# Performance work log

Measured on AMD Instinct MI355X. Metric: run time of the kernel, lower is better.

The kernel has to match this reference:

```python
import jax, jax.numpy as jnp
import numpy as np

EPS = 1e-5  # instance-norm epsilon (NormalizeLayer over spatial axes)

def instance_norm(x):
    # normalize over spatial axes (1,2) per sample, per channel
    mean = jnp.mean(x, axis=(1, 2), keepdims=True)
    var = jnp.var(x, axis=(1, 2), keepdims=True)
    return (x - mean) / jnp.sqrt(var + EPS)

def l2norm(x, axis=-1):
    return x / jnp.sqrt(jnp.sum(x * x, axis=axis, keepdims=True) + 1e-12)

def setup_inputs() -> dict:
    key = jax.random.key(0)
    ks = jax.random.split(key, 5)
    B, H, W, C = 4, 64, 64, 256
    content = jax.random.normal(ks[0], (B, H, W, C), jnp.float32)
    style = jax.random.normal(ks[1], (B, H, W, C), jnp.float32)
    scale = 1.0 / np.sqrt(C)
    Wq = jax.random.normal(ks[2], (C, C), jnp.float32) * scale
    Wk = jax.random.normal(ks[3], (C, C), jnp.float32) * scale
    Wv = jax.random.normal(ks[4], (C, C), jnp.float32) * scale
    bq = jnp.zeros((C,), jnp.float32)
    bk = jnp.zeros((C,), jnp.float32)
    bv = jnp.zeros((C,), jnp.float32)
    return {"content": content, "style": style, "Wq": Wq, "bq": bq,
            "Wk": Wk, "bk": bk, "Wv": Wv, "bv": bv}

def reference(content, style, Wq, bq, Wk, bk, Wv, bv):
    B, H, W, C = content.shape
    N = H * W
    norm_content = instance_norm(content)
    norm_style = instance_norm(style)
    # 1x1 convs == per-pixel linear layers
    Q = (jnp.einsum('bhwc,cd->bhwd', norm_content, Wq) + bq).reshape(B, N, C)
    K = (jnp.einsum('bhwc,cd->bhwd', norm_style, Wk) + bk).reshape(B, N, C)
    V = (jnp.einsum('bhwc,cd->bhwd', style, Wv) + bv).reshape(B, N, C)
    # cosine-similarity attention (Dot with normalize=True)
    attn = jnp.einsum('bnc,bmc->bnm', l2norm(Q), l2norm(K))  # [B, N, N]
    A = jax.nn.softmax(attn, axis=-1)
    M = jnp.einsum('bnm,bmc->bnc', A, V)                 # weighted mean
    S2 = jnp.einsum('bnm,bmc->bnc', A, V * V) - M * M    # weighted variance
    S2 = jax.nn.relu(S2)
    # safe sqrt: grad-safe at exactly 0 (matches sqrt(relu(x)) values)
    S = jnp.where(S2 > 0, jnp.sqrt(jnp.where(S2 > 0, S2, 1.0)), 0.0)
    S = S.reshape(B, H, W, C)
    M = M.reshape(B, H, W, C)
    return S * norm_content + M
```

## Files before the change

### kernel.cpp

```cpp
#include <hip/hip_runtime.h>
#include <cstdint>

#define BB 4
#define NN 4096
#define CC 256

typedef __attribute__((ext_vector_type(8))) short bf16x8;
typedef __attribute__((ext_vector_type(4))) short bf16x4;
typedef __attribute__((ext_vector_type(4))) float f32x4;
typedef unsigned int u32;
typedef __attribute__((ext_vector_type(4))) u32 u32x4;
typedef __attribute__((ext_vector_type(2))) u32 u32x2;

#define MFMA_FP8(a, b, c)  __builtin_amdgcn_mfma_f32_16x16x32_fp8_fp8((a), (b), (c), 0, 0, 0)

#define WAITCNT(vm, xp, lgkm) (((vm) & 0xF) | (((vm) >> 4) << 14) | ((xp) << 4) | ((lgkm) << 8))

__device__ __forceinline__ unsigned short f2bf(float f) {
  union { float f; unsigned u; } v; v.f = f;
  unsigned r = v.u + 0x7fffu + ((v.u >> 16) & 1u);
  return (unsigned short)(r >> 16);
}
__device__ __forceinline__ u32 pk4_fp8(float a, float b, float c, float d) {
  u32 v = (u32)__builtin_amdgcn_cvt_pk_fp8_f32(a, b, 0, false);
  v = (u32)__builtin_amdgcn_cvt_pk_fp8_f32(c, d, (int)v, true);
  return v;
}
__device__ __forceinline__ unsigned char fp8_1(float a) {
  return (unsigned char)(((u32)__builtin_amdgcn_cvt_pk_fp8_f32(a, a, 0, false)) & 0xff);
}

typedef __attribute__((address_space(3))) unsigned int lds_u32;
typedef __attribute__((address_space(1))) unsigned int glb_u32;

__device__ __forceinline__ void async_cp16(const void* g, void* l) {
  __builtin_amdgcn_global_load_lds((const glb_u32*)g,
                                   (lds_u32*)(unsigned)(unsigned long long)l,
                                   16, 0, 0);
}

__global__ __launch_bounds__(256) void transpose_w(const float* __restrict__ Wq,
                                                   const float* __restrict__ Wk,
                                                   const float* __restrict__ Wv,
                                                   unsigned char* __restrict__ Wt8) {
  __shared__ float sT[64 * 65];
  int blk = blockIdx.x;
  int z = blk / 16, tl = blk % 16;
  int c0 = (tl >> 2) * 64, d0 = (tl & 3) * 64;
  const float* W = (z == 0) ? Wq : ((z == 1) ? Wk : Wv);
  #pragma unroll
  for (int i = 0; i < 16; ++i) {
    int e = i * 256 + threadIdx.x;
    int c = e >> 6, d = e & 63;
    sT[c * 65 + d] = W[(size_t)(c0 + c) * CC + d0 + d];
  }
  __syncthreads();
  #pragma unroll
  for (int i = 0; i < 16; ++i) {
    int e = i * 256 + threadIdx.x;
    int d = e >> 6, c = e & 63;
    Wt8[(size_t)z * 65536 + (size_t)(d0 + d) * CC + c0 + c] = fp8_1(sT[c * 65 + d]);
  }
}

__global__ __launch_bounds__(256) void stats_partial(const float* __restrict__ content,
                                                     const float* __restrict__ style,
                                                     float* __restrict__ sums) {
  int blk = blockIdx.x;
  int t = blk >> 9, b = (blk >> 7) & 3, chunk = blk & 127;
  const float* X = t ? style : content;
  int c = threadIdx.x;
  const float* base = X + ((size_t)b * NN + (size_t)chunk * 32) * CC + c;
  float s = 0.f, ss = 0.f;
  #pragma unroll 8
  for (int r = 0; r < 32; ++r) {
    float x = base[(size_t)r * CC];
    s += x; ss += x * x;
  }
  atomicAdd(&sums[((t * 2 + 0) * BB + b) * CC + c], s);
  atomicAdd(&sums[((t * 2 + 1) * BB + b) * CC + c], ss);
}

__global__ __launch_bounds__(256) void stats_finalize(const float* __restrict__ sums,
                                                      float* __restrict__ stats) {
  int i = blockIdx.x * 256 + threadIdx.x;
  int t = i >> 10, bc = i & 1023;
  float s = sums[(t * 2 + 0) * 1024 + bc];
  float ss = sums[(t * 2 + 1) * 1024 + bc];
  float m = s * (1.0f / NN);
  float var = ss * (1.0f / NN) - m * m;
  stats[(t * 2 + 0) * 1024 + bc] = m;
  stats[(t * 2 + 1) * 1024 + bc] = rsqrtf(var + 1e-5f);
}

__global__ __launch_bounds__(256, 2) void qkv_kernel(
    const float* __restrict__ content, const float* __restrict__ style,
    const unsigned char* __restrict__ Wt8,
    const float* __restrict__ bq, const float* __restrict__ bk, const float* __restrict__ bv,
    const float* __restrict__ stats,
    unsigned char* __restrict__ Qn, unsigned char* __restrict__ Kn,
    unsigned char* __restrict__ Vct) {
  __shared__ __align__(16) char sW[32768];
  __shared__ __align__(16) char sX[32768];

  int tid = threadIdx.x;
  int wid = tid >> 6, lane = tid & 63, quad = lane >> 4, l16 = lane & 15;
  int uwid = __builtin_amdgcn_readfirstlane(wid);
  int tileid = blockIdx.x;
  int z = blockIdx.y;
  int gr0 = tileid * 128;
  int b = gr0 >> 12;

  const float* X = (z == 0) ? content : style;
  int statt = (z == 0) ? 0 : 1;
  const float* mean = stats + ((statt * 2 + 0) * BB + b) * CC;
  const float* rstd = stats + ((statt * 2 + 1) * BB + b) * CC;
  bool donorm = (z < 2);

  #pragma unroll
  for (int i = 0; i < 8; ++i) {
    int lin = i * 256 + tid;
    int row = lin >> 4, c16 = lin & 15;
    int c = c16 * 16;
    const float* xr = X + (size_t)(gr0 + row) * CC + c;
    f32x4 x0 = *(const f32x4*)(xr + 0);
    f32x4 x1 = *(const f32x4*)(xr + 4);
    f32x4 x2 = *(const f32x4*)(xr + 8);
    f32x4 x3 = *(const f32x4*)(xr + 12);
    if (donorm) {
      f32x4 m0 = *(const f32x4*)(mean + c + 0), r0 = *(const f32x4*)(rstd + c + 0);
      f32x4 m1 = *(const f32x4*)(mean + c + 4), r1 = *(const f32x4*)(rstd + c + 4);
      f32x4 m2 = *(const f32x4*)(mean + c + 8), r2 = *(const f32x4*)(rstd + c + 8);
      f32x4 m3 = *(const f32x4*)(mean + c + 12), r3 = *(const f32x4*)(rstd + c + 12);
      x0 = (x0 - m0) * r0; x1 = (x1 - m1) * r1;
      x2 = (x2 - m2) * r2; x3 = (x3 - m3) * r3;
    }
    u32x4 pk;
    pk.x = pk4_fp8(x0.x, x0.y, x0.z, x0.w);
    pk.y = pk4_fp8(x1.x, x1.y, x1.z, x1.w);
    pk.z = pk4_fp8(x2.x, x2.y, x2.z, x2.w);
    pk.w = pk4_fp8(x3.x, x3.y, x3.z, x3.w);
    *(u32x4*)(sX + row * 256 + ((c16 ^ (row & 15)) * 16)) = pk;
  }

  f32x4 zero4 = {0.f, 0.f, 0.f, 0.f};
  f32x4 acc[2][16];
  #pragma unroll
  for (int i = 0; i < 2; ++i)
    #pragma unroll
    for (int j = 0; j < 16; ++j) acc[i][j] = zero4;

  const unsigned char* wb = Wt8 + (size_t)z * 65536;

  for (int half = 0; half < 2; ++half) {
    __syncthreads();
    #pragma unroll
    for (int it = 0; it < 8; ++it) {
      int L = it * 256 + wid * 64 + lane;
      int d = L >> 3;
      int c16 = (L & 7) ^ (d & 7);
      async_cp16(wb + (size_t)d * 256 + half * 128 + c16 * 16,
                 sW + (size_t)(it * 256 + uwid * 64) * 16);
    }
    __syncthreads();

    long a[2][4];
    #pragma unroll
    for (int mf = 0; mf < 2; ++mf) {
      int row = wid * 32 + mf * 16 + l16;
      #pragma unroll
      for (int kc = 0; kc < 4; ++kc) {
        int chunk = half * 8 + kc * 2 + (quad >> 1);
        a[mf][kc] = *(const long*)(sX + row * 256 + ((chunk ^ (row & 15)) * 16) + (quad & 1) * 8);
      }
    }
    #pragma unroll
    for (int nf = 0; nf < 16; ++nf) {
      int d = nf * 16 + l16;
      #pragma unroll
      for (int kc = 0; kc < 4; ++kc) {
        long bw = *(const long*)(sW + d * 128 + (((kc * 2 + (quad >> 1)) ^ (d & 7)) * 16) + (quad & 1) * 8);
        acc[0][nf] = MFMA_FP8(a[0][kc], bw, acc[0][nf]);
        acc[1][nf] = MFMA_FP8(a[1][kc], bw, acc[1][nf]);
      }
    }
  }

  const float* bias = (z == 0) ? bq : ((z == 1) ? bk : bv);
  #pragma unroll
  for (int nf = 0; nf < 16; ++nf) {
    float bb_ = bias[nf * 16 + l16];
    #pragma unroll
    for (int mf = 0; mf < 2; ++mf) {
      acc[mf][nf].x += bb_; acc[mf][nf].y += bb_;
      acc[mf][nf].z += bb_; acc[mf][nf].w += bb_;
    }
  }

  if (z < 2) {
    unsigned char* O = (z == 0) ? Qn : Kn;
    #pragma unroll
    for (int mf = 0; mf < 2; ++mf) {
      f32x4 ss = zero4;
      #pragma unroll
      for (int nf = 0; nf < 16; ++nf) ss += acc[mf][nf] * acc[mf][nf];
      #pragma unroll
      for (int m = 1; m < 16; m <<= 1) {
        ss.x += __shfl_xor(ss.x, m, 64);
        ss.y += __shfl_xor(ss.y, m, 64);
        ss.z += __shfl_xor(ss.z, m, 64);
        ss.w += __shfl_xor(ss.w, m, 64);
      }
      f32x4 rq;
      rq.x = rsqrtf(ss.x + 1e-12f); rq.y = rsqrtf(ss.y + 1e-12f);
      rq.z = rsqrtf(ss.z + 1e-12f); rq.w = rsqrtf(ss.w + 1e-12f);
      int r0 = wid * 32 + mf * 16 + quad * 4;
      #pragma unroll
      for (int nf = 0; nf < 16; ++nf) {
        int col = nf * 16 + l16;
        u32 p01 = (u32)__builtin_amdgcn_cvt_pk_fp8_f32(acc[mf][nf].x * rq.x, acc[mf][nf].y * rq.y, 0, false);
        u32 p23 = (u32)__builtin_amdgcn_cvt_pk_fp8_f32(acc[mf][nf].z * rq.z, acc[mf][nf].w * rq.w, 0, false);
        O[(size_t)(gr0 + r0 + 0) * CC + col] = (unsigned char)(p01 & 0xff);
        O[(size_t)(gr0 + r0 + 1) * CC + col] = (unsigned char)((p01 >> 8) & 0xff);
        O[(size_t)(gr0 + r0 + 2) * CC + col] = (unsigned char)(p23 & 0xff);
        O[(size_t)(gr0 + r0 + 3) * CC + col] = (unsigned char)((p23 >> 8) & 0xff);
      }
    }
  } else {
    char* sOT = sX;
    int n_in_b = gr0 & (NN - 1);
    int ktbase = n_in_b >> 6;
    __syncthreads();
    #pragma unroll
    for (int pass = 0; pass < 2; ++pass) {
      #pragma unroll
      for (int mf = 0; mf < 2; ++mf) {
        int j = wid * 2 + mf;
        #pragma unroll
        for (int nf = 0; nf < 16; ++nf) {
          int col = nf * 16 + l16;
          f32x4 v = acc[mf][nf];
          f32x4 w = pass ? (v * v) : v;
          u32 pk = pk4_fp8(w.x, w.y, w.z, w.w);
          *(u32*)(sOT + col * 128 + ((j ^ (col & 7)) * 16) + quad * 4) = pk;
        }
      }
      __syncthreads();
      int ch = pass * 256 + tid;
      unsigned char* vb = Vct + (size_t)b * 2097152 + (size_t)ch * 8;
      #pragma unroll
      for (int j = 0; j < 8; ++j) {
        u32x4 val = *(const u32x4*)(sOT + tid * 128 + ((j ^ (tid & 7)) * 16));
        int ktile = ktbase + (j >> 2);
        int ks = (j >> 1) & 1;
        int q0 = (j & 1) * 2;
        unsigned char* basep = vb + (size_t)((ktile * 2 + ks) * 4 + q0) * 4096;
        u32x2 lo; lo.x = val.x; lo.y = val.y;
        u32x2 hi; hi.x = val.z; hi.y = val.w;
        *(u32x2*)(basep) = lo;
        *(u32x2*)(basep + 4096) = hi;
      }
      __syncthreads();
    }
  }
}

__global__ __launch_bounds__(512, 4) void flash_kernel(
    const unsigned char* __restrict__ Qn,
    const unsigned char* __restrict__ Kn,
    const unsigned char* __restrict__ Vct,
    const float* __restrict__ content,
    const float* __restrict__ stats,
    float* __restrict__ out) {
  __shared__ __align__(16) char smem[32768 + 4096 + 128];
  char* sKb = smem;
  char* sPb = smem + 32768;
  float* sL = (float*)(smem + 36864);
  float* sE2 = (float*)smem;

  int tid = threadIdx.x;
  int wid = tid >> 6, lane = tid & 63, quad = lane >> 4, l16 = lane & 15;
  int uwid = __builtin_amdgcn_readfirstlane(wid);

  int id = blockIdx.x;
  int b = (id >> 1) & 3;
  int tile = ((id >> 3) << 1) | (id & 1);
  int q0 = tile * 32;

  int qh = (wid >> 2) * 16;
  int kb0 = (wid & 3) * 16;
  int cw = wid * 64;

  long qf[8];
  {
    int row = q0 + qh + l16;
    const unsigned char* base = Qn + (((size_t)b * NN + row) << 8);
    #pragma unroll
    for (int kf = 0; kf < 8; ++kf)
      qf[kf] = *(const long*)(base + kf * 32 + quad * 8);
  }
  __builtin_amdgcn_s_waitcnt(WAITCNT(0, 7, 15));

  if (tid < 32) sL[tid] = 0.f;

  const unsigned char* kbp = Kn + (((size_t)b * NN) << 8);
  const unsigned char* vbp = Vct + (size_t)b * 2097152 + quad * 4096 + (size_t)(cw + l16) * 8;

  auto stageK = [&](int k0, int buf) {
    char* dst = sKb + buf * 16384;
    #pragma unroll
    for (int it = 0; it < 2; ++it) {
      int L = it * 512 + wid * 64 + lane;
      int ky = L >> 4, s = L & 15;
      int c16 = s ^ (ky & 15);
      async_cp16(kbp + (((size_t)(k0 + ky)) << 8) + c16 * 16,
                 dst + (size_t)(it * 512 + uwid * 64) * 16);
    }
  };

  f32x4 zero4 = {0.f, 0.f, 0.f, 0.f};
  f32x4 om[2][4];
  #pragma unroll
  for (int i = 0; i < 2; ++i)
    #pragma unroll
    for (int j = 0; j < 4; ++j) om[i][j] = zero4;
  float Lr = 0.f;
  long vf[2][4];

  int krow = kb0 + l16;
  int krowoff = krow * 256;
  int khalf = (quad & 1) * 8;

  auto s_phase = [&](int kt) {
    const char* sKc = sKb + (kt & 1) * 16384;
    char* sPc = sPb + (kt & 1) * 2048;
    f32x4 ta = zero4, tb = zero4;
    #pragma unroll
    for (int kf = 0; kf < 8; kf += 2) {
      int sa = (kf * 2 + (quad >> 1)) ^ (krow & 15);
      long aka = *(const long*)(sKc + krowoff + sa * 16 + khalf);
      ta = MFMA_FP8(aka, qf[kf], ta);
      int sb = ((kf + 1) * 2 + (quad >> 1)) ^ (krow & 15);
      long akb = *(const long*)(sKc + krowoff + sb * 16 + khalf);
      tb = MFMA_FP8(akb, qf[kf + 1], tb);
    }
    f32x4 sv = ta + tb;
    float p0 = __expf(sv.x), p1 = __expf(sv.y), p2 = __expf(sv.z), p3 = __expf(sv.w);
    Lr += p0 + p1 + p2 + p3;
    u32 w = pk4_fp8(p0, p1, p2, p3);
    int q = qh + l16;
    int c = (kb0 >> 2) + quad;
    *(u32*)(sPc + q * 64 + ((c ^ (q & 14)) * 4)) = w;
    const unsigned char* vt = vbp + (size_t)kt * 32768;
    #pragma unroll
    for (int ks = 0; ks < 2; ++ks)
      #pragma unroll
      for (int nf = 0; nf < 4; ++nf)
        vf[ks][nf] = *(const long*)(vt + ks * 16384 + nf * 128);
  };

  stageK(0, 0);  stageK(64, 1);
  __builtin_amdgcn_s_waitcnt(WAITCNT(2, 7, 15));
  __builtin_amdgcn_s_barrier();
  s_phase(0);
  __builtin_amdgcn_s_waitcnt(WAITCNT(63, 7, 0));
  __builtin_amdgcn_s_barrier();

  for (int kt = 0; kt < 64; ++kt) {
    stageK(((kt + 2) & 63) * 64, kt & 1);

    __builtin_amdgcn_s_waitcnt(WAITCNT(2, 7, 15));

    const char* sPc = sPb + (kt & 1) * 2048;
    long pf[2][2];
    #pragma unroll
    for (int ks = 0; ks < 2; ++ks)
      #pragma unroll
      for (int mf = 0; mf < 2; ++mf) {
        int q = mf * 16 + l16;
        int c = ks * 8 + quad * 2;
        pf[ks][mf] = *(const long*)(sPc + q * 64 + ((c ^ (q & 14)) * 4));
      }

    #pragma unroll
    for (int ks = 0; ks < 2; ++ks)
      #pragma unroll
      for (int nf = 0; nf < 4; ++nf)
        #pragma unroll
        for (int mf = 0; mf < 2; ++mf)
          om[mf][nf] = MFMA_FP8(pf[ks][mf], vf[ks][nf], om[mf][nf]);

    if (kt < 63) s_phase(kt + 1);

    __builtin_amdgcn_s_waitcnt(WAITCNT(63, 7, 0));
    __builtin_amdgcn_s_barrier();
  }

  Lr += __shfl_xor(Lr, 16, 64);
  Lr += __shfl_xor(Lr, 32, 64);
  if (quad == 0) atomicAdd(&sL[qh + l16], Lr);
  __builtin_amdgcn_s_waitcnt(WAITCNT(0, 7, 0));
  __builtin_amdgcn_s_barrier();

  if (wid >= 4) {
    #pragma unroll
    for (int mf = 0; mf < 2; ++mf) {
      #pragma unroll
      for (int nf = 0; nf < 4; ++nf) {
        int ch = (wid - 4) * 64 + nf * 16 + l16;
        int cidx = (mf * 4 + quad) ^ (ch & 7);
        *(f32x4*)(sE2 + ch * 32 + cidx * 4) = om[mf][nf];
      }
    }
  }
  __syncthreads();

  if (wid < 4) {
    const float* meanc = stats + (0 * BB + b) * CC;
    const float* rstdc = stats + (1 * BB + b) * CC;
    float linv[2][4];
    #pragma unroll
    for (int mf = 0; mf < 2; ++mf)
      #pragma unroll
      for (int r = 0; r < 4; ++r)
        linv[mf][r] = 1.0f / sL[mf * 16 + quad * 4 + r];
    #pragma unroll
    for (int nf = 0; nf < 4; ++nf) {
      int ch = cw + nf * 16 + l16;
      float mc = meanc[ch], rc = rstdc[ch];
      #pragma unroll
      for (int mf = 0; mf < 2; ++mf) {
        int cidx = (mf * 4 + quad) ^ (ch & 7);
        f32x4 vv = *(const f32x4*)(sE2 + ch * 32 + cidx * 4);
        f32x4 ov = om[mf][nf];
        #pragma unroll
        for (int r = 0; r < 4; ++r) {
          int row = mf * 16 + quad * 4 + r;
          float li = linv[mf][r];
          float ovr = (r == 0) ? ov.x : (r == 1) ? ov.y : (r == 2) ? ov.z : ov.w;
          float vvr = (r == 0) ? vv.x : (r == 1) ? vv.y : (r == 2) ? vv.z : vv.w;
          float M = ovr * li;
          float E2 = vvr * li;
          float S2 = E2 - M * M;
          float S = (S2 > 0.f) ? sqrtf(S2) : 0.f;
          size_t gi = (((size_t)b * NN + q0 + row) << 8) + ch;
          float xh = (content[gi] - mc) * rc;
          out[gi] = S * xh + M;
        }
      }
    }
  }
}

extern "C" void kernel_launch(void* const* d_in, const int* in_sizes, int n_in,
                              void* d_out, int out_size, void* d_ws, size_t ws_size,
                              hipStream_t stream) {
  const float* content = (const float*)d_in[0];
  const float* style   = (const float*)d_in[1];
  const float* Wq = (const float*)d_in[2];
  const float* bq = (const float*)d_in[3];
  const float* Wk = (const float*)d_in[4];
  const float* bk = (const float*)d_in[5];
  const float* Wv = (const float*)d_in[6];
  const float* bv = (const float*)d_in[7];
  char* ws = (char*)d_ws;

  float* sums        = (float*)(ws + 0);
  float* stats       = (float*)(ws + 16384);
  unsigned char* Wt8 = (unsigned char*)(ws + 32768);
  unsigned char* Qn  = (unsigned char*)(ws + 229376);
  unsigned char* Kn  = (unsigned char*)(ws + 4423680);
  unsigned char* Vct = (unsigned char*)(ws + 8617984);
  float* outp = (float*)d_out;

  hipMemsetAsync(d_ws, 0, 16384, stream);
  hipLaunchKernelGGL(transpose_w, dim3(48), dim3(256), 0, stream, Wq, Wk, Wv, Wt8);
  hipLaunchKernelGGL(stats_partial, dim3(1024), dim3(256), 0, stream, content, style, sums);
  hipLaunchKernelGGL(stats_finalize, dim3(8), dim3(256), 0, stream, sums, stats);
  hipLaunchKernelGGL(qkv_kernel, dim3(128, 3), dim3(256), 0, stream,
                     content, style, Wt8, bq, bk, bv, stats, Qn, Kn, Vct);
  hipLaunchKernelGGL(flash_kernel, dim3(512), dim3(512), 0, stream,
                     Qn, Kn, Vct, content, stats, outp);
}
```

Baseline: 206.7 us.

## Split flash attention over key halves with a separate reduction kernel

```diff
diff --git a/kernel.cpp b/kernel.cpp
--- a/kernel.cpp
+++ b/kernel.cpp
@@ -265,7 +265,7 @@
   }
 }
 
-__global__ __launch_bounds__(512, 4) void flash_kernel(
+__global__ __launch_bounds__(512, 4) void flash_fused(
     const unsigned char* __restrict__ Qn,
     const unsigned char* __restrict__ Kn,
     const unsigned char* __restrict__ Vct,
@@ -368,7 +368,6 @@
 
   for (int kt = 0; kt < 64; ++kt) {
     stageK(((kt + 2) & 63) * 64, kt & 1);
-
     __builtin_amdgcn_s_waitcnt(WAITCNT(2, 7, 15));
 
     const char* sPc = sPb + (kt & 1) * 2048;
@@ -452,6 +451,190 @@
   }
 }
 
+__global__ __launch_bounds__(512, 8) void flash_split(
+    const unsigned char* __restrict__ Qn,
+    const unsigned char* __restrict__ Kn,
+    const unsigned char* __restrict__ Vct,
+    float* __restrict__ gOM,
+    float* __restrict__ gL) {
+  __shared__ __align__(16) char smem[32768 + 4096 + 128];
+  char* sKb = smem;
+  char* sPb = smem + 32768;
+  float* sL = (float*)(smem + 36864);
+
+  int tid = threadIdx.x;
+  int wid = tid >> 6, lane = tid & 63, quad = lane >> 4, l16 = lane & 15;
+  int uwid = __builtin_amdgcn_readfirstlane(wid);
+
+  int id = blockIdx.x;
+  int kh = id >> 9;
+  int b = (id >> 1) & 3;
+  int tile = (((id & 511) >> 3) << 1) | (id & 1);
+  int q0 = tile * 32;
+  int kt0 = kh << 5;
+
+  int qh = (wid >> 2) * 16;
+  int kb0 = (wid & 3) * 16;
+  int cw = wid * 64;
+
+  long qf[8];
+  {
+    int row = q0 + qh + l16;
+    const unsigned char* base = Qn + (((size_t)b * NN + row) << 8);
+    #pragma unroll
+    for (int kf = 0; kf < 8; ++kf)
+      qf[kf] = *(const long*)(base + kf * 32 + quad * 8);
+  }
+  __builtin_amdgcn_s_waitcnt(WAITCNT(0, 7, 15));
+
+  if (tid < 32) sL[tid] = 0.f;
+
+  const unsigned char* kbp = Kn + (((size_t)b * NN) << 8);
+  const unsigned char* vbp = Vct + (size_t)b * 2097152 + quad * 4096 + (size_t)(cw + l16) * 8;
+
+  auto stageK = [&](int k0, int buf) {
+    char* dst = sKb + buf * 16384;
+    #pragma unroll
+    for (int it = 0; it < 2; ++it) {
+      int L = it * 512 + wid * 64 + lane;
+      int ky = L >> 4, s = L & 15;
+      int c16 = s ^ (ky & 15);
+      async_cp16(kbp + (((size_t)(k0 + ky)) << 8) + c16 * 16,
+                 dst + (size_t)(it * 512 + uwid * 64) * 16);
+    }
+  };
+
+  f32x4 zero4 = {0.f, 0.f, 0.f, 0.f};
+  f32x4 om[2][4];
+  #pragma unroll
+  for (int i = 0; i < 2; ++i)
+    #pragma unroll
+    for (int j = 0; j < 4; ++j) om[i][j] = zero4;
+  float Lr = 0.f;
+  long vf[2][4];
+
+  int krow = kb0 + l16;
+  int krowoff = krow * 256;
+  int khalf = (quad & 1) * 8;
+
+  auto s_phase = [&](int kt) {
+    const char* sKc = sKb + (kt & 1) * 16384;
+    char* sPc = sPb + (kt & 1) * 2048;
+    f32x4 ta = zero4, tb = zero4;
+    #pragma unroll
+    for (int kf = 0; kf < 8; kf += 2) {
+      int sa = (kf * 2 + (quad >> 1)) ^ (krow & 15);
+      long aka = *(const long*)(sKc + krowoff + sa * 16 + khalf);
+      ta = MFMA_FP8(aka, qf[kf], ta);
+      int sb = ((kf + 1) * 2 + (quad >> 1)) ^ (krow & 15);
+      long akb = *(const long*)(sKc + krowoff + sb * 16 + khalf);
+      tb = MFMA_FP8(akb, qf[kf + 1], tb);
+    }
+    f32x4 sv = ta + tb;
+    float p0 = __expf(sv.x), p1 = __expf(sv.y), p2 = __expf(sv.z), p3 = __expf(sv.w);
+    Lr += p0 + p1 + p2 + p3;
+    u32 w = pk4_fp8(p0, p1, p2, p3);
+    int q = qh + l16;
+    int c = (kb0 >> 2) + quad;
+    *(u32*)(sPc + q * 64 + ((c ^ (q & 14)) * 4)) = w;
+    const unsigned char* vt = vbp + (size_t)kt * 32768;
+    #pragma unroll
+    for (int ks = 0; ks < 2; ++ks)
+      #pragma unroll
+      for (int nf = 0; nf < 4; ++nf)
+        vf[ks][nf] = *(const long*)(vt + ks * 16384 + nf * 128);
+  };
+
+  stageK(kt0 * 64, 0);  stageK((kt0 + 1) * 64, 1);
+  __builtin_amdgcn_s_waitcnt(WAITCNT(2, 7, 15));
+  __builtin_amdgcn_s_barrier();
+  s_phase(kt0);
+  __builtin_amdgcn_s_waitcnt(WAITCNT(63, 7, 0));
+  __builtin_amdgcn_s_barrier();
+
+  for (int i = 0; i < 32; ++i) {
+    int kt = kt0 + i;
+    stageK(((kt + 2) & 63) * 64, kt & 1);
+    __builtin_amdgcn_s_waitcnt(WAITCNT(2, 7, 15));
+
+    const char* sPc = sPb + (kt & 1) * 2048;
+    long pf[2][2];
+    #pragma unroll
+    for (int ks = 0; ks < 2; ++ks)
+      #pragma unroll
+      for (int mf = 0; mf < 2; ++mf) {
+        int q = mf * 16 + l16;
+        int c = ks * 8 + quad * 2;
+        pf[ks][mf] = *(const long*)(sPc + q * 64 + ((c ^ (q & 14)) * 4));
+      }
+
+    #pragma unroll
+    for (int ks = 0; ks < 2; ++ks)
+      #pragma unroll
+      for (int nf = 0; nf < 4; ++nf)
+        #pragma unroll
+        for (int mf = 0; mf < 2; ++mf)
+          om[mf][nf] = MFMA_FP8(pf[ks][mf], vf[ks][nf], om[mf][nf]);
+
+    if (i < 31) s_phase(kt + 1);
+
+    __builtin_amdgcn_s_waitcnt(WAITCNT(63, 7, 0));
+    __builtin_amdgcn_s_barrier();
+  }
+
+  Lr += __shfl_xor(Lr, 16, 64);
+  Lr += __shfl_xor(Lr, 32, 64);
+  if (quad == 0) atomicAdd(&sL[qh + l16], Lr);
+  __builtin_amdgcn_s_waitcnt(WAITCNT(0, 7, 0));
+  __builtin_amdgcn_s_barrier();
+
+  int tb2 = (b * 128 + tile) * 2 + kh;
+  if (tid < 32) gL[tb2 * 32 + tid] = sL[tid];
+  float* gb = gOM + (size_t)tb2 * (32 * 512);
+  #pragma unroll
+  for (int mf = 0; mf < 2; ++mf) {
+    int qrow = mf * 16 + quad * 4;
+    #pragma unroll
+    for (int nf = 0; nf < 4; ++nf) {
+      int ch = cw + nf * 16 + l16;
+      f32x4 v = om[mf][nf];
+      gb[(size_t)(qrow + 0) * 512 + ch] = v.x;
+      gb[(size_t)(qrow + 1) * 512 + ch] = v.y;
+      gb[(size_t)(qrow + 2) * 512 + ch] = v.z;
+      gb[(size_t)(qrow + 3) * 512 + ch] = v.w;
+    }
+  }
+}
+
+__global__ __launch_bounds__(256) void reduce_kernel(
+    const float* __restrict__ gOM, const float* __restrict__ gL,
+    const float* __restrict__ content, const float* __restrict__ stats,
+    float* __restrict__ out) {
+  int bx = blockIdx.x;
+  int qh2 = blockIdx.y;
+  int b = bx >> 7, tile = bx & 127;
+  int t = threadIdx.x;
+  __shared__ float sLr[32];
+  if (t < 32) sLr[t] = gL[(bx * 2 + 0) * 32 + t] + gL[(bx * 2 + 1) * 32 + t];
+  __syncthreads();
+  float mc = stats[(0 * BB + b) * CC + t];
+  float rc = stats[(1 * BB + b) * CC + t];
+  const float* g0 = gOM + (size_t)(bx * 2 + 0) * (32 * 512);
+  const float* g1 = gOM + (size_t)(bx * 2 + 1) * (32 * 512);
+  #pragma unroll 4
+  for (int qq = 0; qq < 16; ++qq) {
+    int q = qh2 * 16 + qq;
+    float li = 1.0f / sLr[q];
+    float M  = (g0[(size_t)q * 512 + t]       + g1[(size_t)q * 512 + t])       * li;
+    float E2 = (g0[(size_t)q * 512 + 256 + t] + g1[(size_t)q * 512 + 256 + t]) * li;
+    float S2 = E2 - M * M;
+    float S = (S2 > 0.f) ? sqrtf(S2) : 0.f;
+    size_t gi = (((size_t)b * NN + tile * 32 + q) << 8) + t;
+    float xh = (content[gi] - mc) * rc;
+    out[gi] = S * xh + M;
+  }
+}
+
 extern "C" void kernel_launch(void* const* d_in, const int* in_sizes, int n_in,
                               void* d_out, int out_size, void* d_ws, size_t ws_size,
                               hipStream_t stream) {
@@ -471,6 +654,9 @@
   unsigned char* Qn  = (unsigned char*)(ws + 229376);
   unsigned char* Kn  = (unsigned char*)(ws + 4423680);
   unsigned char* Vct = (unsigned char*)(ws + 8617984);
+  float* gL          = (float*)(ws + 17006592);
+  float* gOM         = (float*)(ws + 17137664);
+  const size_t WS_NEED = 17137664ull + 67108864ull;
   float* outp = (float*)d_out;
 
   hipMemsetAsync(d_ws, 0, 16384, stream);
@@ -479,6 +665,13 @@
   hipLaunchKernelGGL(stats_finalize, dim3(8), dim3(256), 0, stream, sums, stats);
   hipLaunchKernelGGL(qkv_kernel, dim3(128, 3), dim3(256), 0, stream,
                      content, style, Wt8, bq, bk, bv, stats, Qn, Kn, Vct);
-  hipLaunchKernelGGL(flash_kernel, dim3(512), dim3(512), 0, stream,
-                     Qn, Kn, Vct, content, stats, outp);
-}
+  if (ws_size >= WS_NEED) {
+    hipLaunchKernelGGL(flash_split, dim3(1024), dim3(512), 0, stream,
+                       Qn, Kn, Vct, gOM, gL);
+    hipLaunchKernelGGL(reduce_kernel, dim3(512, 2), dim3(256), 0, stream,
+                       gOM, gL, content, stats, outp);
+  } else {
+    hipLaunchKernelGGL(flash_fused, dim3(512), dim3(512), 0, stream,
+                       Qn, Kn, Vct, content, stats, outp);
+  }
+}
```

Measured after the change: 429.8 us. 2.08x slower.
